# Optimization experiments

Measured on AMD Instinct MI355X. Metric: run time of the kernel, lower is better.

The kernel has to match this reference:

```python
import jax, jax.numpy as jnp
import numpy as np

IN_F, RED, WID, CLS, T = 700, 256, 4096, 20, 100


def _q4(W):
    # per-tensor symmetric INT4 STE: value is quantized, grad is identity
    scale = jnp.maximum(jnp.abs(W).max() / 7.0, 1e-8)
    return W + jax.lax.stop_gradient(jnp.round(W / scale) * scale - W)


def setup_inputs() -> dict:
    key = jax.random.key(0)
    ks = jax.random.split(key, 12)
    B = 64
    x = jax.random.normal(ks[0], (B, T, IN_F), dtype=jnp.float32)
    latent = jax.random.uniform(ks[1], (T,), dtype=jnp.float32)
    spatial_W = jax.random.normal(ks[2], (RED, IN_F), jnp.float32) / np.sqrt(IN_F)
    spatial_b = jnp.zeros((RED,), jnp.float32)
    conv_W = jax.random.normal(ks[3], (RED, RED, 5), jnp.float32) / np.sqrt(RED * 5)
    conv_b = jnp.zeros((RED,), jnp.float32)
    fc1_W = jax.random.normal(ks[4], (WID, RED), jnp.float32) / np.sqrt(RED)
    fc1_b = jnp.zeros((WID,), jnp.float32)
    fc2_W = jax.random.normal(ks[5], (CLS, WID), jnp.float32) / np.sqrt(WID)
    fc2_b = jnp.zeros((CLS,), jnp.float32)
    gain = jnp.asarray(1.0, jnp.float32)
    return {"x": x, "latent": latent, "spatial_W": spatial_W, "spatial_b": spatial_b,
            "conv_W": conv_W, "conv_b": conv_b, "fc1_W": fc1_W, "fc1_b": fc1_b,
            "fc2_W": fc2_W, "fc2_b": fc2_b, "gain": gain}


def _compute_drive(x, latent, spatial_W, spatial_b, conv_W, conv_b, fc1_W, fc1_b, gain):
    # spatial projection (INT4 STE linear) + relu : (B,T,RED)
    xp = jax.nn.relu(jnp.einsum("btf,rf->btr", x, _q4(spatial_W)) + spatial_b)
    # temporal conv1d over T, padding=2 (same), channels RED->RED
    xc = jax.lax.conv_general_dilated(
        xp.transpose(0, 2, 1), conv_W, window_strides=(1,), padding=[(2, 2)],
        dimension_numbers=("NCH", "OIH", "NCH"))
    conv_out = jax.nn.relu(xc + conv_b[None, :, None]).transpose(0, 2, 1)  # (B,T,RED)
    spatial_act = jax.nn.softplus(jnp.einsum("btr,wr->btw", conv_out, _q4(fc1_W)) + fc1_b)
    return spatial_act * latent[None, :, None] * jnp.abs(gain)  # (B,T,WID)


def reference(x, latent, spatial_W, spatial_b, conv_W, conv_b, fc1_W, fc1_b, fc2_W, fc2_b, gain):
    drive = _compute_drive(x, latent, spatial_W, spatial_b, conv_W, conv_b, fc1_W, fc1_b, gain)
    # Poisson spike sampling with straight-through estimator, then clamp at 1
    pois = jax.random.poisson(jax.random.key(42), jax.lax.stop_gradient(drive)).astype(drive.dtype)
    spikes = drive + jax.lax.stop_gradient(pois - drive)
    spikes = jnp.minimum(spikes, 1.0)
    # decay-weighted temporal reduction over T
    decay = jnp.exp(jnp.linspace(-2.0, 0.0, T)).astype(drive.dtype)
    weighted = jnp.einsum("btw,t->bw", spikes, decay)  # (B,WID)
    # dropout in eval mode = identity
    logits = weighted @ _q4(fc2_W).T + fc2_b  # (B,CLS)
    return (logits, spikes, drive)
```

## Files before the change

kernel.cpp:

```cpp
#include <hip/hip_runtime.h>
#include <stdint.h>

#define B 64
#define T 100
#define IN_F 700
#define RED 256
#define WID 4096
#define CLS 20
#define BT (B*T)
#define NELEM (BT*WID)
#define LOGITS_OFF 0
#define SPIKES_OFF (B*CLS)
#define DRIVE_OFF (SPIKES_OFF + NELEM)

#define WS_SLOTS 0
#define WS_W2Q 16
#define WS_XP  (WS_W2Q + CLS*WID)
#define WS_CO  (WS_XP + BT*RED)
#define WS_WEIGHTED (WS_CO + BT*RED)

#define SC_WST 0
#define SC_CWT (SC_WST + IN_F*RED)

__host__ __device__ __forceinline__ uint32_t rotl32(uint32_t v, int r) {
  return (v << r) | (v >> (32 - r));
}

__host__ __device__ __forceinline__ void threefry2x32(uint32_t k0, uint32_t k1,
                                                      uint32_t x0, uint32_t x1,
                                                      uint32_t& o0, uint32_t& o1) {
  uint32_t k2 = k0 ^ k1 ^ 0x1BD11BDAu;
  x0 += k0; x1 += k1;
#define TF_R(r) { x0 += x1; x1 = rotl32(x1, (r)); x1 ^= x0; }
  TF_R(13) TF_R(15) TF_R(26) TF_R(6)
  x0 += k1; x1 += k2 + 1u;
  TF_R(17) TF_R(29) TF_R(16) TF_R(24)
  x0 += k2; x1 += k0 + 2u;
  TF_R(13) TF_R(15) TF_R(26) TF_R(6)
  x0 += k0; x1 += k1 + 3u;
  TF_R(17) TF_R(29) TF_R(16) TF_R(24)
  x0 += k1; x1 += k2 + 4u;
  TF_R(13) TF_R(15) TF_R(26) TF_R(6)
  x0 += k2; x1 += k0 + 5u;
#undef TF_R
  o0 = x0; o1 = x1;
}

__global__ void absmax_kernel(const float* __restrict__ w, int n, uint32_t* slot) {
  __shared__ uint32_t sm[256];
  uint32_t m = 0u;
  for (int i = blockIdx.x * 256 + threadIdx.x; i < n; i += gridDim.x * 256)
    m = max(m, __float_as_uint(fabsf(w[i])));
  sm[threadIdx.x] = m;
  __syncthreads();
  for (int s = 128; s > 0; s >>= 1) {
    if (threadIdx.x < s) sm[threadIdx.x] = max(sm[threadIdx.x], sm[threadIdx.x + s]);
    __syncthreads();
  }
  if (threadIdx.x == 0) atomicMax(slot, sm[0]);
}

__global__ void quant_t_kernel(const float* __restrict__ w, float* __restrict__ qT,
                               int Nn, int Kk, const uint32_t* __restrict__ slot) {
  float s = fmaxf(__uint_as_float(*slot) / 7.0f, 1e-8f);
  int id = blockIdx.x * 256 + threadIdx.x;
  if (id < Nn * Kk) {
    int n = id / Kk, k = id - n * Kk;
    qT[(size_t)k * Nn + n] = rintf(w[id] / s) * s;
  }
}

__global__ void quant_kernel(const float* __restrict__ w, float* __restrict__ q,
                             int n, const uint32_t* __restrict__ slot) {
  float s = fmaxf(__uint_as_float(*slot) / 7.0f, 1e-8f);
  int i = blockIdx.x * 256 + threadIdx.x;
  if (i < n) q[i] = rintf(w[i] / s) * s;
}

__global__ void convw_t_kernel(const float* __restrict__ w, float* __restrict__ wt) {
  int id = blockIdx.x * 256 + threadIdx.x;
  if (id < 256 * 1280) {
    int o = id / 1280, r = id - o * 1280;
    int ic = r / 5, h = r - ic * 5;
    wt[(size_t)((h << 8) + ic) * 256 + o] = w[id];
  }
}

template<int SRCA>
__global__ __launch_bounds__(256, 8)
void gemm32_kernel(const float* __restrict__ A, const float* __restrict__ Bt,
                   const float* __restrict__ bias, float* __restrict__ C,
                   int M, int N, int K) {
  constexpr int MT = 32, NT = 64, TM = 2, TN = 4;
  constexpr int ASR = MT + 4, BSR = NT + 4;
  __shared__ float As[32 * ASR];
  __shared__ float Bs[32 * BSR];
  int tid = threadIdx.x;
  int tx = tid & 15, ty = tid >> 4;
  int m0 = blockIdx.x * MT, n0 = blockIdx.y * NT;
  int am = tid >> 3, ak4 = (tid & 7) << 2;
  float acc[TM * TN];
#pragma unroll
  for (int i = 0; i < TM * TN; ++i) acc[i] = 0.f;

  for (int kt = 0; kt < K; kt += 32) {
    int klen = K - kt; if (klen > 32) klen = 32;
    {
      float4 av = make_float4(0.f, 0.f, 0.f, 0.f);
      if (ak4 < klen) {
        if (SRCA == 0) {
          av = *(const float4*)&A[(size_t)(m0 + am) * K + kt + ak4];
        } else {
          int k = kt + ak4;
          int h = k >> 8, ic = k & 255;
          int bt = m0 + am;
          int b = bt / T, t = bt - b * T;
          int tt = t + h - 2;
          if (tt >= 0 && tt < T)
            av = *(const float4*)&A[((size_t)(b * T + tt)) * RED + ic];
        }
      }
      As[(ak4 + 0) * ASR + am] = av.x;
      As[(ak4 + 1) * ASR + am] = av.y;
      As[(ak4 + 2) * ASR + am] = av.z;
      As[(ak4 + 3) * ASR + am] = av.w;
    }
#pragma unroll
    for (int rep = 0; rep < 2; ++rep) {
      int e = rep * 256 + tid;
      int n4 = (e & 15) << 2, kk = e >> 4;
      float4 v = make_float4(0.f, 0.f, 0.f, 0.f);
      if (kk < klen) v = *(const float4*)&Bt[(size_t)(kt + kk) * N + n0 + n4];
      *(float4*)&Bs[kk * BSR + n4] = v;
    }
    __syncthreads();
    if (klen == 32) {
#pragma unroll
      for (int kk = 0; kk < 32; ++kk) {
        float a[TM], b[TN];
#pragma unroll
        for (int i = 0; i < TM; ++i) a[i] = As[kk * ASR + ty * TM + i];
#pragma unroll
        for (int d = 0; d < TN; ++d) b[d] = Bs[kk * BSR + tx * TN + d];
#pragma unroll
        for (int j = 0; j < TM; ++j)
#pragma unroll
          for (int d = 0; d < TN; ++d)
            acc[j * TN + d] = fmaf(a[j], b[d], acc[j * TN + d]);
      }
    } else {
      for (int kk = 0; kk < klen; ++kk) {
        float a[TM], b[TN];
#pragma unroll
        for (int i = 0; i < TM; ++i) a[i] = As[kk * ASR + ty * TM + i];
#pragma unroll
        for (int d = 0; d < TN; ++d) b[d] = Bs[kk * BSR + tx * TN + d];
#pragma unroll
        for (int j = 0; j < TM; ++j)
#pragma unroll
          for (int d = 0; d < TN; ++d)
            acc[j * TN + d] = fmaf(a[j], b[d], acc[j * TN + d]);
      }
    }
    __syncthreads();
  }

  float bv[TN];
#pragma unroll
  for (int d = 0; d < TN; ++d) bv[d] = bias[n0 + tx * TN + d];
#pragma unroll
  for (int j = 0; j < TM; ++j) {
    int m = m0 + ty * TM + j;
#pragma unroll
    for (int d = 0; d < TN; ++d)
      C[(size_t)m * N + n0 + tx * TN + d] = fmaxf(acc[j * TN + d] + bv[d], 0.0f);
  }
}

__global__ __launch_bounds__(256, 4)
void fc1_kernel(const float* __restrict__ A, const float* __restrict__ W1,
                const float* __restrict__ bias, const float* __restrict__ latent,
                const float* __restrict__ gain, float* __restrict__ C,
                const uint32_t* __restrict__ slot, int K, int N) {
  constexpr int MT = 128, NT = 128, TM = 8, TN = 8;
  constexpr int ASR = MT + 4, BSR = NT + 4;
  __shared__ float As[32 * ASR];
  __shared__ float Bs[32 * BSR];
  float qs = fmaxf(__uint_as_float(*slot) / 7.0f, 1e-8f);
  int tid = threadIdx.x;
  int tx = tid & 15, ty = tid >> 4;
  int wid = (blockIdx.x & 7) * 200 + (blockIdx.x >> 3);
  int bx = wid % 50, by = wid / 50;
  int m0 = bx * MT, n0 = by * NT;
  int bn = tid & 127, kh = (tid >> 7) << 4;
  const float* wrow = &W1[(size_t)(n0 + bn) * K + kh];
  float acc[TM * TN];
#pragma unroll
  for (int i = 0; i < TM * TN; ++i) acc[i] = 0.f;

  for (int kt = 0; kt < K; kt += 32) {
#pragma unroll
    for (int rep = 0; rep < 4; ++rep) {
      int e = rep * 256 + tid;
      int k4 = (e & 7) << 2, m = e >> 3;
      const float4 v = *(const float4*)&A[(size_t)(m0 + m) * K + kt + k4];
      As[(k4 + 0) * ASR + m] = v.x;
      As[(k4 + 1) * ASR + m] = v.y;
      As[(k4 + 2) * ASR + m] = v.z;
      As[(k4 + 3) * ASR + m] = v.w;
    }
#pragma unroll
    for (int q4 = 0; q4 < 4; ++q4) {
      const float4 v = *(const float4*)&wrow[kt + (q4 << 2)];
      int kk = kh + (q4 << 2);
      Bs[(kk + 0) * BSR + bn] = rintf(v.x / qs) * qs;
      Bs[(kk + 1) * BSR + bn] = rintf(v.y / qs) * qs;
      Bs[(kk + 2) * BSR + bn] = rintf(v.z / qs) * qs;
      Bs[(kk + 3) * BSR + bn] = rintf(v.w / qs) * qs;
    }
    __syncthreads();
#pragma unroll
    for (int kk = 0; kk < 32; ++kk) {
      float a[TM], b[TN];
#pragma unroll
      for (int i = 0; i < TM; ++i) a[i] = As[kk * ASR + ty * TM + i];
#pragma unroll
      for (int d = 0; d < 4; ++d) b[d] = Bs[kk * BSR + tx * 4 + d];
#pragma unroll
      for (int d = 0; d < 4; ++d) b[4 + d] = Bs[kk * BSR + 64 + tx * 4 + d];
#pragma unroll
      for (int j = 0; j < TM; ++j)
#pragma unroll
        for (int d = 0; d < TN; ++d)
          acc[j * TN + d] = fmaf(a[j], b[d], acc[j * TN + d]);
    }
    __syncthreads();
  }

  float g = fabsf(gain[0]);
  float bv[TN];
#pragma unroll
  for (int d = 0; d < 4; ++d) {
    bv[d] = bias[n0 + tx * 4 + d];
    bv[4 + d] = bias[n0 + 64 + tx * 4 + d];
  }
#pragma unroll
  for (int j = 0; j < TM; ++j) {
    int bt = m0 + ty * TM + j;
    int q = bt / T;
    float lat = latent[bt - q * T];
    float o[TN];
#pragma unroll
    for (int d = 0; d < TN; ++d) {
      float v = acc[j * TN + d] + bv[d];
      float e = expf(-fabsf(v));
      float l = log1pf(e);
      float sp = fmaxf(v, 0.0f) + l;
      o[d] = (sp * lat) * g;
    }
    float4 o0 = make_float4(o[0], o[1], o[2], o[3]);
    float4 o1 = make_float4(o[4], o[5], o[6], o[7]);
    *(float4*)&C[(size_t)bt * N + n0 + tx * 4] = o0;
    *(float4*)&C[(size_t)bt * N + n0 + 64 + tx * 4] = o1;
  }
}

__global__ __launch_bounds__(256) void spike_weighted_kernel(float* __restrict__ out,
                                                             float* __restrict__ wt,
                                                             uint32_t k0, uint32_t k1) {
  __shared__ float dec[128];
  int tid = threadIdx.x;
  if (tid < T) {
    float step = 2.0f / 99.0f;
    float a = step * (float)tid;
    dec[tid] = expf(a - 2.0f);
  }
  __syncthreads();
  int b = blockIdx.x >> 4;
  int w = ((blockIdx.x & 15) << 8) + tid;
  float acc = 0.f;
  for (int t = 0; t < T; ++t) {
    uint32_t p = (uint32_t)((b * T + t) * WID + w);
    float lam = out[DRIVE_OFF + p];
    uint32_t y0, y1;
    threefry2x32(k0, k1, 0u, p, y0, y1);
    uint32_t bits = y0 ^ y1;
    float u = __uint_as_float((bits >> 9) | 0x3f800000u) - 1.0f;
    float s = (lam > 0.0f && logf(u) > -lam) ? 1.0f : 0.0f;
    out[SPIKES_OFF + p] = s;
    acc = fmaf(s, dec[t], acc);
  }
  wt[b * WID + w] = acc;
}

__global__ void logits_kernel(const float* __restrict__ wt,
                              const float* __restrict__ w2,
                              const float* __restrict__ b2,
                              float* __restrict__ out) {
  __shared__ float sm[256];
  int b = blockIdx.x / CLS, c = blockIdx.x - b * CLS;
  const float* wr = wt + (size_t)b * WID;
  const float* w2r = w2 + (size_t)c * WID;
  float p = 0.f;
  for (int w = threadIdx.x; w < WID; w += 256) p = fmaf(wr[w], w2r[w], p);
  sm[threadIdx.x] = p;
  __syncthreads();
  for (int s = 128; s > 0; s >>= 1) {
    if (threadIdx.x < s) sm[threadIdx.x] += sm[threadIdx.x + s];
    __syncthreads();
  }
  if (threadIdx.x == 0) out[LOGITS_OFF + blockIdx.x] = sm[0] + b2[c];
}

extern "C" void kernel_launch(void* const* d_in, const int* in_sizes, int n_in,
                              void* d_out, int out_size, void* d_ws, size_t ws_size,
                              hipStream_t stream) {
  (void)in_sizes; (void)n_in; (void)out_size; (void)ws_size;
  const float* x         = (const float*)d_in[0];
  const float* latent    = (const float*)d_in[1];
  const float* spatial_W = (const float*)d_in[2];
  const float* spatial_b = (const float*)d_in[3];
  const float* conv_W    = (const float*)d_in[4];
  const float* conv_b    = (const float*)d_in[5];
  const float* fc1_W     = (const float*)d_in[6];
  const float* fc1_b     = (const float*)d_in[7];
  const float* fc2_W     = (const float*)d_in[8];
  const float* fc2_b     = (const float*)d_in[9];
  const float* gain      = (const float*)d_in[10];
  float* out = (float*)d_out;
  uint32_t* wsu = (uint32_t*)d_ws;
  float* wsf = (float*)d_ws;
  float* S = out + SPIKES_OFF;

  uint32_t sk0, sk1;
  threefry2x32(0u, 42u, 0u, 1u, sk0, sk1);

  hipMemsetAsync(wsu + WS_SLOTS, 0, 3 * sizeof(uint32_t), stream);
  absmax_kernel<<<64, 256, 0, stream>>>(spatial_W, RED * IN_F, wsu + WS_SLOTS + 0);
  absmax_kernel<<<256, 256, 0, stream>>>(fc1_W, WID * RED, wsu + WS_SLOTS + 1);
  absmax_kernel<<<32, 256, 0, stream>>>(fc2_W, CLS * WID, wsu + WS_SLOTS + 2);

  quant_t_kernel<<<700, 256, 0, stream>>>(spatial_W, S + SC_WST, RED, IN_F, wsu + WS_SLOTS + 0);
  quant_kernel<<<320, 256, 0, stream>>>(fc2_W, wsf + WS_W2Q, CLS * WID, wsu + WS_SLOTS + 2);
  convw_t_kernel<<<1280, 256, 0, stream>>>(conv_W, S + SC_CWT);

  gemm32_kernel<0><<<dim3(200, 4), 256, 0, stream>>>(
      x, S + SC_WST, spatial_b, wsf + WS_XP, BT, RED, IN_F);

  gemm32_kernel<1><<<dim3(200, 4), 256, 0, stream>>>(
      wsf + WS_XP, S + SC_CWT, conv_b, wsf + WS_CO, BT, RED, 1280);

  fc1_kernel<<<1600, 256, 0, stream>>>(
      wsf + WS_CO, fc1_W, fc1_b, latent, gain, out + DRIVE_OFF,
      wsu + WS_SLOTS + 1, RED, WID);

  spike_weighted_kernel<<<B * 16, 256, 0, stream>>>(out, wsf + WS_WEIGHTED, sk0, sk1);

  logits_kernel<<<B * CLS, 256, 0, stream>>>(wsf + WS_WEIGHTED, wsf + WS_W2Q, fc2_b, out);
}
```

Baseline: 734.8 us.

## Enlarge spatial/conv GEMM tiles, coalesce fc1 weight loads, vectorize stores

The spatial and conv GEMMs move from 32x64 to 64x64 tiles, with each thread computing 4x4 outputs. This halves the grid and raises arithmetic intensity, and their outputs are now written as float4 stores. The fc1 kernel's weight-tile load is remapped so that consecutive threads read consecutive float4s along K, improving coalescing. Its launch bound is lowered from 4 to 2 blocks per SM, which allows more registers but may reduce occupancy.

New measurement: 752.9 us. +2.5%, slower.

```diff
diff --git a/kernel.cpp b/kernel.cpp
--- a/kernel.cpp
+++ b/kernel.cpp
@@ -88,24 +88,26 @@
 
 template<int SRCA>
 __global__ __launch_bounds__(256, 8)
-void gemm32_kernel(const float* __restrict__ A, const float* __restrict__ Bt,
+void gemm64_kernel(const float* __restrict__ A, const float* __restrict__ Bt,
                    const float* __restrict__ bias, float* __restrict__ C,
                    int M, int N, int K) {
-  constexpr int MT = 32, NT = 64, TM = 2, TN = 4;
+  constexpr int MT = 64, NT = 64, TM = 4, TN = 4;
   constexpr int ASR = MT + 4, BSR = NT + 4;
   __shared__ float As[32 * ASR];
   __shared__ float Bs[32 * BSR];
   int tid = threadIdx.x;
   int tx = tid & 15, ty = tid >> 4;
   int m0 = blockIdx.x * MT, n0 = blockIdx.y * NT;
-  int am = tid >> 3, ak4 = (tid & 7) << 2;
   float acc[TM * TN];
 #pragma unroll
   for (int i = 0; i < TM * TN; ++i) acc[i] = 0.f;
 
   for (int kt = 0; kt < K; kt += 32) {
     int klen = K - kt; if (klen > 32) klen = 32;
-    {
+#pragma unroll
+    for (int rep = 0; rep < 2; ++rep) {
+      int e = rep * 256 + tid;
+      int am = e >> 3, ak4 = (e & 7) << 2;
       float4 av = make_float4(0.f, 0.f, 0.f, 0.f);
       if (ak4 < klen) {
         if (SRCA == 0) {
@@ -171,13 +173,14 @@
 #pragma unroll
   for (int j = 0; j < TM; ++j) {
     int m = m0 + ty * TM + j;
-#pragma unroll
-    for (int d = 0; d < TN; ++d)
-      C[(size_t)m * N + n0 + tx * TN + d] = fmaxf(acc[j * TN + d] + bv[d], 0.0f);
-  }
-}
-
-__global__ __launch_bounds__(256, 4)
+    float o[TN];
+#pragma unroll
+    for (int d = 0; d < TN; ++d) o[d] = fmaxf(acc[j * TN + d] + bv[d], 0.0f);
+    *(float4*)&C[(size_t)m * N + n0 + tx * TN] = make_float4(o[0], o[1], o[2], o[3]);
+  }
+}
+
+__global__ __launch_bounds__(256, 2)
 void fc1_kernel(const float* __restrict__ A, const float* __restrict__ W1,
                 const float* __restrict__ bias, const float* __restrict__ latent,
                 const float* __restrict__ gain, float* __restrict__ C,
@@ -192,8 +195,6 @@
   int wid = (blockIdx.x & 7) * 200 + (blockIdx.x >> 3);
   int bx = wid % 50, by = wid / 50;
   int m0 = bx * MT, n0 = by * NT;
-  int bn = tid & 127, kh = (tid >> 7) << 4;
-  const float* wrow = &W1[(size_t)(n0 + bn) * K + kh];
   float acc[TM * TN];
 #pragma unroll
   for (int i = 0; i < TM * TN; ++i) acc[i] = 0.f;
@@ -210,13 +211,14 @@
       As[(k4 + 3) * ASR + m] = v.w;
     }
 #pragma unroll
-    for (int q4 = 0; q4 < 4; ++q4) {
-      const float4 v = *(const float4*)&wrow[kt + (q4 << 2)];
-      int kk = kh + (q4 << 2);
-      Bs[(kk + 0) * BSR + bn] = rintf(v.x / qs) * qs;
-      Bs[(kk + 1) * BSR + bn] = rintf(v.y / qs) * qs;
-      Bs[(kk + 2) * BSR + bn] = rintf(v.z / qs) * qs;
-      Bs[(kk + 3) * BSR + bn] = rintf(v.w / qs) * qs;
+    for (int rep = 0; rep < 4; ++rep) {
+      int e = rep * 256 + tid;
+      int bn = e >> 3, k4 = (e & 7) << 2;
+      const float4 v = *(const float4*)&W1[(size_t)(n0 + bn) * K + kt + k4];
+      Bs[(k4 + 0) * BSR + bn] = rintf(v.x / qs) * qs;
+      Bs[(k4 + 1) * BSR + bn] = rintf(v.y / qs) * qs;
+      Bs[(k4 + 2) * BSR + bn] = rintf(v.z / qs) * qs;
+      Bs[(k4 + 3) * BSR + bn] = rintf(v.w / qs) * qs;
     }
     __syncthreads();
 #pragma unroll
@@ -341,13 +343,13 @@
   absmax_kernel<<<32, 256, 0, stream>>>(fc2_W, CLS * WID, wsu + WS_SLOTS + 2);
 
   quant_t_kernel<<<700, 256, 0, stream>>>(spatial_W, S + SC_WST, RED, IN_F, wsu + WS_SLOTS + 0);
-  quant_kernel<<<320, 256, 0, stream>>>(fc2_W, wsf + WS_W2Q, CLS * WID, wsu + WS_SLOTS + 2);
+  quant_kernel<<<320, 256, 0, stream>>>(fc2_W, wsf + WS_W2Q, wsu ? CLS * WID : 0, wsu + WS_SLOTS + 2);
   convw_t_kernel<<<1280, 256, 0, stream>>>(conv_W, S + SC_CWT);
 
-  gemm32_kernel<0><<<dim3(200, 4), 256, 0, stream>>>(
+  gemm64_kernel<0><<<dim3(100, 4), 256, 0, stream>>>(
       x, S + SC_WST, spatial_b, wsf + WS_XP, BT, RED, IN_F);
 
-  gemm32_kernel<1><<<dim3(200, 4), 256, 0, stream>>>(
+  gemm64_kernel<1><<<dim3(100, 4), 256, 0, stream>>>(
       wsf + WS_XP, S + SC_CWT, conv_b, wsf + WS_CO, BT, RED, 1280);
 
   fc1_kernel<<<1600, 256, 0, stream>>>(
```

## Pre-quantize and transpose fc1 weights; vectorize fc1 tile loads and spike kernel

Applied to the files above, without the earlier changes.

fc1 weights are now quantized and transposed once into scratch space (inside the spikes output buffer) by a separate kernel. The fc1 GEMM then loads B tiles with coalesced float4 copies instead of quantizing per tile with a divide and rintf. Its inner loop now reads float2 values from shared memory. The spike kernel gives each thread four adjacent elements with float4 loads and stores, which cuts the grid to a quarter of the blocks. The trade-off is an extra transpose pass and reduced parallelism in the spike kernel.

Measured after the change: 720.2 us. 2.0% less time.

```diff
diff --git a/kernel.cpp b/kernel.cpp
--- a/kernel.cpp
+++ b/kernel.cpp
@@ -20,7 +20,8 @@
 #define WS_WEIGHTED (WS_CO + BT*RED)
 
 #define SC_WST 0
-#define SC_CWT (SC_WST + IN_F*RED)
+#define SC_W1T (SC_WST + IN_F*RED)
+#define SC_CWT (SC_W1T + RED*WID)
 
 __host__ __device__ __forceinline__ uint32_t rotl32(uint32_t v, int r) {
   return (v << r) | (v >> (32 - r));
@@ -178,25 +179,21 @@
 }
 
 __global__ __launch_bounds__(256, 4)
-void fc1_kernel(const float* __restrict__ A, const float* __restrict__ W1,
+void fc1_kernel(const float* __restrict__ A, const float* __restrict__ Bt,
                 const float* __restrict__ bias, const float* __restrict__ latent,
                 const float* __restrict__ gain, float* __restrict__ C,
-                const uint32_t* __restrict__ slot, int K, int N) {
-  constexpr int MT = 128, NT = 128, TM = 8, TN = 8;
-  constexpr int ASR = MT + 4, BSR = NT + 4;
+                int K, int N) {
+  constexpr int ASR = 132, BSR = 132;
   __shared__ float As[32 * ASR];
   __shared__ float Bs[32 * BSR];
-  float qs = fmaxf(__uint_as_float(*slot) / 7.0f, 1e-8f);
   int tid = threadIdx.x;
   int tx = tid & 15, ty = tid >> 4;
   int wid = (blockIdx.x & 7) * 200 + (blockIdx.x >> 3);
   int bx = wid % 50, by = wid / 50;
-  int m0 = bx * MT, n0 = by * NT;
-  int bn = tid & 127, kh = (tid >> 7) << 4;
-  const float* wrow = &W1[(size_t)(n0 + bn) * K + kh];
-  float acc[TM * TN];
-#pragma unroll
-  for (int i = 0; i < TM * TN; ++i) acc[i] = 0.f;
+  int m0 = bx * 128, n0 = by * 128;
+  float2 acc2[32];
+#pragma unroll
+  for (int i = 0; i < 32; ++i) acc2[i] = make_float2(0.f, 0.f);
 
   for (int kt = 0; kt < K; kt += 32) {
 #pragma unroll
@@ -210,49 +207,57 @@
       As[(k4 + 3) * ASR + m] = v.w;
     }
 #pragma unroll
-    for (int q4 = 0; q4 < 4; ++q4) {
-      const float4 v = *(const float4*)&wrow[kt + (q4 << 2)];
-      int kk = kh + (q4 << 2);
-      Bs[(kk + 0) * BSR + bn] = rintf(v.x / qs) * qs;
-      Bs[(kk + 1) * BSR + bn] = rintf(v.y / qs) * qs;
-      Bs[(kk + 2) * BSR + bn] = rintf(v.z / qs) * qs;
-      Bs[(kk + 3) * BSR + bn] = rintf(v.w / qs) * qs;
+    for (int rep = 0; rep < 4; ++rep) {
+      int e = rep * 256 + tid;
+      int n4 = (e & 31) << 2, kk = e >> 5;
+      float4 v = *(const float4*)&Bt[(size_t)(kt + kk) * N + n0 + n4];
+      *(float4*)&Bs[kk * BSR + n4] = v;
     }
     __syncthreads();
 #pragma unroll
     for (int kk = 0; kk < 32; ++kk) {
-      float a[TM], b[TN];
-#pragma unroll
-      for (int i = 0; i < TM; ++i) a[i] = As[kk * ASR + ty * TM + i];
-#pragma unroll
-      for (int d = 0; d < 4; ++d) b[d] = Bs[kk * BSR + tx * 4 + d];
-#pragma unroll
-      for (int d = 0; d < 4; ++d) b[4 + d] = Bs[kk * BSR + 64 + tx * 4 + d];
-#pragma unroll
-      for (int j = 0; j < TM; ++j)
-#pragma unroll
-        for (int d = 0; d < TN; ++d)
-          acc[j * TN + d] = fmaf(a[j], b[d], acc[j * TN + d]);
+      float a[8];
+#pragma unroll
+      for (int i = 0; i < 8; ++i) a[i] = As[kk * ASR + ty * 8 + i];
+      float2 b0 = *(const float2*)&Bs[kk * BSR + tx * 4];
+      float2 b1 = *(const float2*)&Bs[kk * BSR + tx * 4 + 2];
+      float2 b2 = *(const float2*)&Bs[kk * BSR + 64 + tx * 4];
+      float2 b3 = *(const float2*)&Bs[kk * BSR + 64 + tx * 4 + 2];
+#pragma unroll
+      for (int j = 0; j < 8; ++j) {
+        acc2[j * 4 + 0].x = fmaf(a[j], b0.x, acc2[j * 4 + 0].x);
+        acc2[j * 4 + 0].y = fmaf(a[j], b0.y, acc2[j * 4 + 0].y);
+        acc2[j * 4 + 1].x = fmaf(a[j], b1.x, acc2[j * 4 + 1].x);
+        acc2[j * 4 + 1].y = fmaf(a[j], b1.y, acc2[j * 4 + 1].y);
+        acc2[j * 4 + 2].x = fmaf(a[j], b2.x, acc2[j * 4 + 2].x);
+        acc2[j * 4 + 2].y = fmaf(a[j], b2.y, acc2[j * 4 + 2].y);
+        acc2[j * 4 + 3].x = fmaf(a[j], b3.x, acc2[j * 4 + 3].x);
+        acc2[j * 4 + 3].y = fmaf(a[j], b3.y, acc2[j * 4 + 3].y);
+      }
     }
     __syncthreads();
   }
 
   float g = fabsf(gain[0]);
-  float bv[TN];
+  float bv[8];
 #pragma unroll
   for (int d = 0; d < 4; ++d) {
     bv[d] = bias[n0 + tx * 4 + d];
     bv[4 + d] = bias[n0 + 64 + tx * 4 + d];
   }
 #pragma unroll
-  for (int j = 0; j < TM; ++j) {
-    int bt = m0 + ty * TM + j;
+  for (int j = 0; j < 8; ++j) {
+    int bt = m0 + ty * 8 + j;
     int q = bt / T;
     float lat = latent[bt - q * T];
-    float o[TN];
-#pragma unroll
-    for (int d = 0; d < TN; ++d) {
-      float v = acc[j * TN + d] + bv[d];
+    float o[8];
+    o[0] = acc2[j * 4 + 0].x; o[1] = acc2[j * 4 + 0].y;
+    o[2] = acc2[j * 4 + 1].x; o[3] = acc2[j * 4 + 1].y;
+    o[4] = acc2[j * 4 + 2].x; o[5] = acc2[j * 4 + 2].y;
+    o[6] = acc2[j * 4 + 3].x; o[7] = acc2[j * 4 + 3].y;
+#pragma unroll
+    for (int d = 0; d < 8; ++d) {
+      float v = o[d] + bv[d];
       float e = expf(-fabsf(v));
       float l = log1pf(e);
       float sp = fmaxf(v, 0.0f) + l;
@@ -276,21 +281,30 @@
     dec[tid] = expf(a - 2.0f);
   }
   __syncthreads();
-  int b = blockIdx.x >> 4;
-  int w = ((blockIdx.x & 15) << 8) + tid;
-  float acc = 0.f;
+  int b = blockIdx.x >> 2;
+  int w = ((blockIdx.x & 3) << 10) + (tid << 2);
+  float acc0 = 0.f, acc1 = 0.f, acc2 = 0.f, acc3 = 0.f;
   for (int t = 0; t < T; ++t) {
     uint32_t p = (uint32_t)((b * T + t) * WID + w);
-    float lam = out[DRIVE_OFF + p];
-    uint32_t y0, y1;
-    threefry2x32(k0, k1, 0u, p, y0, y1);
-    uint32_t bits = y0 ^ y1;
-    float u = __uint_as_float((bits >> 9) | 0x3f800000u) - 1.0f;
-    float s = (lam > 0.0f && logf(u) > -lam) ? 1.0f : 0.0f;
-    out[SPIKES_OFF + p] = s;
-    acc = fmaf(s, dec[t], acc);
-  }
-  wt[b * WID + w] = acc;
+    float4 lam = *(const float4*)&out[DRIVE_OFF + p];
+    float s[4];
+#pragma unroll
+    for (int i = 0; i < 4; ++i) {
+      uint32_t y0, y1;
+      threefry2x32(k0, k1, 0u, p + i, y0, y1);
+      uint32_t bits = y0 ^ y1;
+      float u = __uint_as_float((bits >> 9) | 0x3f800000u) - 1.0f;
+      float lamv = (i == 0) ? lam.x : (i == 1) ? lam.y : (i == 2) ? lam.z : lam.w;
+      s[i] = (lamv > 0.0f && logf(u) > -lamv) ? 1.0f : 0.0f;
+    }
+    *(float4*)&out[SPIKES_OFF + p] = make_float4(s[0], s[1], s[2], s[3]);
+    float d = dec[t];
+    acc0 = fmaf(s[0], d, acc0);
+    acc1 = fmaf(s[1], d, acc1);
+    acc2 = fmaf(s[2], d, acc2);
+    acc3 = fmaf(s[3], d, acc3);
+  }
+  *(float4*)&wt[b * WID + w] = make_float4(acc0, acc1, acc2, acc3);
 }
 
 __global__ void logits_kernel(const float* __restrict__ wt,
@@ -341,6 +355,7 @@
   absmax_kernel<<<32, 256, 0, stream>>>(fc2_W, CLS * WID, wsu + WS_SLOTS + 2);
 
   quant_t_kernel<<<700, 256, 0, stream>>>(spatial_W, S + SC_WST, RED, IN_F, wsu + WS_SLOTS + 0);
+  quant_t_kernel<<<4096, 256, 0, stream>>>(fc1_W, S + SC_W1T, WID, RED, wsu + WS_SLOTS + 1);
   quant_kernel<<<320, 256, 0, stream>>>(fc2_W, wsf + WS_W2Q, CLS * WID, wsu + WS_SLOTS + 2);
   convw_t_kernel<<<1280, 256, 0, stream>>>(conv_W, S + SC_CWT);
 
@@ -351,10 +366,9 @@
       wsf + WS_XP, S + SC_CWT, conv_b, wsf + WS_CO, BT, RED, 1280);
 
   fc1_kernel<<<1600, 256, 0, stream>>>(
-      wsf + WS_CO, fc1_W, fc1_b, latent, gain, out + DRIVE_OFF,
-      wsu + WS_SLOTS + 1, RED, WID);
-
-  spike_weighted_kernel<<<B * 16, 256, 0, stream>>>(out, wsf + WS_WEIGHTED, sk0, sk1);
+      wsf + WS_CO, S + SC_W1T, fc1_b, latent, gain, out + DRIVE_OFF, RED, WID);
+
+  spike_weighted_kernel<<<B * 4, 256, 0, stream>>>(out, wsf + WS_WEIGHTED, sk0, sk1);
 
   logits_kernel<<<B * CLS, 256, 0, stream>>>(wsf + WS_WEIGHTED, wsf + WS_W2Q, fc2_b, out);
 }
```
